# Kernel tuning notes

Measured on AMD Instinct MI355X. Metric: run time of the kernel, lower is better.

The kernel has to match this reference:

```python
import jax, jax.numpy as jnp
import numpy as np

B, S, H, DH = 4, 2048, 16, 64
D = H * DH          # 1024
EXP = 2
FF_IN = EXP * D * 2  # 4096 (SwiGLU doubles)
FF_HID = EXP * D     # 2048
SCALE_BASE = 512
LN_EPS = 1e-5


def setup_inputs() -> dict:
    key = jax.random.key(0)
    ks = jax.random.split(key, 8)
    inp = {
        "q": jax.random.normal(ks[0], (B, S, D), jnp.float32),
        "k": jax.random.normal(ks[1], (B, S, D), jnp.float32),
        "v": jax.random.normal(ks[2], (B, S, D), jnp.float32),
        "Wqkv": jax.random.normal(ks[3], (D, 3 * D), jnp.float32) * (1.0 / np.sqrt(D)),
        "bqkv": jnp.zeros((3 * D,), jnp.float32),
        "q_scale": jnp.ones((DH,), jnp.float32),
        "k_scale": jnp.ones((DH,), jnp.float32),
        "ln_g": jnp.ones((D,), jnp.float32),
        "ln_b": jnp.zeros((D,), jnp.float32),
        "W1": jax.random.normal(ks[4], (D, FF_IN), jnp.float32) * (1.0 / np.sqrt(D)),
        "b1": jnp.zeros((FF_IN,), jnp.float32),
        "W2": jax.random.normal(ks[5], (FF_HID, D), jnp.float32) * (1.0 / np.sqrt(FF_HID)),
        "b2": jnp.zeros((D,), jnp.float32),
    }
    return inp


def rotate_half(x):
    x1, x2 = jnp.split(x, 2, axis=-1)
    return jnp.concatenate((-x2, x1), axis=-1)


def apply_rope(pos, t, scale):
    # pos: [S, DH], scale: [S, DH] (broadcast over [B, H, S, DH])
    return t * jnp.cos(pos) * scale + rotate_half(t) * jnp.sin(pos) * scale


def rotary_tables(seq_len):
    inv_freq = 1.0 / (10000.0 ** (jnp.arange(0, DH, 2, dtype=jnp.float32) / DH))
    t = jnp.arange(seq_len, dtype=jnp.float32)
    freqs = t[:, None] * inv_freq[None, :]            # [S, DH/2]
    freqs = jnp.concatenate((freqs, freqs), axis=-1)  # [S, DH]
    power = (t - seq_len // 2) / SCALE_BASE           # [S]
    base = (jnp.arange(0, DH, 2, dtype=jnp.float32) + 0.4 * DH) / (1.4 * DH)  # [DH/2]
    scale = base[None, :] ** power[:, None]           # [S, DH/2]
    scale = jnp.concatenate((scale, scale), axis=-1)  # [S, DH]
    return freqs, scale


def l2norm(x, eps=1e-12):
    n = jnp.sqrt(jnp.sum(x * x, axis=-1, keepdims=True))
    return x / jnp.maximum(n, eps)


def reference(q, k, v, Wqkv, bqkv, q_scale, k_scale, ln_g, ln_b, W1, b1, W2, b2):
    del k, v  # module projects qkv from q; k,v args are unused (faithful to source)
    n, seq_len, _ = q.shape
    qkv = q @ Wqkv + bqkv                              # [B, S, 3D]
    qkv = qkv.reshape(n, seq_len, H, 3 * DH).transpose(0, 2, 1, 3)  # [B, H, S, 3DH]
    q_, k_, v_ = jnp.split(qkv, 3, axis=-1)
    q_ = l2norm(q_) * q_scale
    k_ = l2norm(k_) * k_scale
    pos, xscale = rotary_tables(seq_len)
    q_ = apply_rope(pos, q_, xscale)
    k_ = apply_rope(pos, k_, 1.0 / xscale)
    # scaled dot product attention (non-causal)
    scores = jnp.einsum("bhid,bhjd->bhij", q_, k_) / np.sqrt(DH)
    attn = jax.nn.softmax(scores, axis=-1)
    out = jnp.einsum("bhij,bhjd->bhid", attn, v_)      # [B, H, S, DH]
    out = out.transpose(0, 2, 1, 3).reshape(n, seq_len, D)
    # LayerNorm
    mu = jnp.mean(out, axis=-1, keepdims=True)
    var = jnp.mean((out - mu) ** 2, axis=-1, keepdims=True)
    out = (out - mu) / jnp.sqrt(var + LN_EPS) * ln_g + ln_b
    # SwiGLU FFN (dropout = identity in eval)
    h = out @ W1 + b1                                  # [B, S, FF_IN]
    x_, gate = jnp.split(h, 2, axis=-1)
    ff = (jax.nn.silu(gate) * x_) @ W2 + b2            # [B, S, D]
    return out + ff
```

## Files before the change

kernel.cpp:

```cpp
#include <hip/hip_runtime.h>
#include <math.h>


typedef __bf16 bf16;
typedef bf16 bf16x8 __attribute__((ext_vector_type(8)));
typedef bf16 bf16x4 __attribute__((ext_vector_type(4)));
typedef float f32x4 __attribute__((ext_vector_type(4)));

#define MFMA(a, b, c) __builtin_amdgcn_mfma_f32_16x16x32_bf16(a, b, c, 0, 0, 0)

__device__ __forceinline__ void async16(const void* g, void* l) {
    __builtin_amdgcn_global_load_lds(
        (const __attribute__((address_space(1))) void*)g,
        (__attribute__((address_space(3))) void*)l,
        16, 0, 0);
}

__global__ __launch_bounds__(256) void fill_sentinel(float* __restrict__ o)
{
    size_t i = ((size_t)blockIdx.x * 256 + threadIdx.x) * 4;
    *(float4*)&o[i] = make_float4(0.25f, 0.25f, 0.25f, 0.25f);
}

__global__ __launch_bounds__(256) void convert_f32_bf16(
    const float* __restrict__ in, bf16* __restrict__ out)
{
    size_t i = ((size_t)blockIdx.x * 256 + threadIdx.x) * 8;
    float4 f0 = *(const float4*)&in[i];
    float4 f1 = *(const float4*)&in[i + 4];
    bf16x8 v;
    v[0] = (bf16)f0.x; v[1] = (bf16)f0.y; v[2] = (bf16)f0.z; v[3] = (bf16)f0.w;
    v[4] = (bf16)f1.x; v[5] = (bf16)f1.y; v[6] = (bf16)f1.z; v[7] = (bf16)f1.w;
    *(bf16x8*)&out[i] = v;
}

__global__ __launch_bounds__(256) void transpose_f32_bf16(
    const float* __restrict__ in, bf16* __restrict__ out, int K, int N)
{
    __shared__ bf16 T[64][70];
    const int tN = N >> 6;
    const int tk = blockIdx.x / tN, tn = blockIdx.x % tN;
    const int k0 = tk << 6, n0 = tn << 6;
    const int t = threadIdx.x;
    const int r = t >> 2, c0 = (t & 3) << 4;
    const float* src = &in[(size_t)(k0 + r) * N + n0 + c0];
    for (int j = 0; j < 4; ++j) {
        float4 f = *(const float4*)(src + 4 * j);
        T[r][c0 + 4 * j + 0] = (bf16)f.x;
        T[r][c0 + 4 * j + 1] = (bf16)f.y;
        T[r][c0 + 4 * j + 2] = (bf16)f.z;
        T[r][c0 + 4 * j + 3] = (bf16)f.w;
    }
    __syncthreads();
    bf16x8 o0, o1;
    for (int i = 0; i < 8; ++i) o0[i] = T[c0 + i][r];
    for (int i = 0; i < 8; ++i) o1[i] = T[c0 + 8 + i][r];
    *(bf16x8*)&out[(size_t)(n0 + r) * K + k0 + c0]     = o0;
    *(bf16x8*)&out[(size_t)(n0 + r) * K + k0 + c0 + 8] = o1;
}

__global__ __launch_bounds__(256) void transpose_v(
    const bf16* __restrict__ in, bf16* __restrict__ out)
{
    __shared__ bf16 T[64][72];
    const int bh = blockIdx.x >> 5;
    const int s0 = (blockIdx.x & 31) << 6;
    const bf16* ip = in + ((size_t)bh << 17) + (size_t)s0 * 64;
    bf16* op = out + ((size_t)bh << 17) + s0;
    const int t = threadIdx.x;
    const int r = t >> 2, c0 = (t & 3) << 4;
    *(bf16x8*)&T[r][c0]     = *(const bf16x8*)&ip[r * 64 + c0];
    *(bf16x8*)&T[r][c0 + 8] = *(const bf16x8*)&ip[r * 64 + c0 + 8];
    __syncthreads();
    bf16x8 o0, o1;
    for (int i = 0; i < 8; ++i) o0[i] = T[c0 + i][r];
    for (int i = 0; i < 8; ++i) o1[i] = T[c0 + 8 + i][r];
    *(bf16x8*)&op[(size_t)r * 2048 + c0]     = o0;
    *(bf16x8*)&op[(size_t)r * 2048 + c0 + 8] = o1;
}

template <int BN>
__device__ __forceinline__ void g256_stage(
    const bf16* __restrict__ Ag, const bf16* __restrict__ Bg, int kt,
    int lda, int K, char* aB, char* bB, int tid, int wave)
{
    for (int i = 0; i < 4; ++i) {
        int l = (i << 9) + tid;
        int r = l >> 3;
        int cbs = ((l & 7) ^ (r & 7)) << 3;
        int cu = (i << 9) + (wave << 6);
        async16(&Ag[(size_t)r * lda + kt + cbs], aB + (size_t)cu * 16);
    }
    for (int i = 0; i < BN / 64; ++i) {
        int l = (i << 9) + tid;
        int r = l >> 3;
        int cbs = ((l & 7) ^ (r & 7)) << 3;
        int cu = (i << 9) + (wave << 6);
        async16(&Bg[(size_t)r * K + kt + cbs], bB + (size_t)cu * 16);
    }
}

template <int NI>
__device__ __forceinline__ void g256_compute(
    const bf16* At, const bf16* Bt, f32x4 (&acc)[8][NI],
    int wm, int wn, int l16, int quad, int rsw)
{
    for (int kd = 0; kd < 2; ++kd) {
        bf16x8 af[8], bfr[NI];
        for (int mi = 0; mi < 8; ++mi) {
            int row = (wm << 7) + (mi << 4) + l16;
            af[mi] = *(const bf16x8*)&At[(row << 6) + ((((kd << 2) + quad) ^ rsw) << 3)];
        }
        for (int ni = 0; ni < NI; ++ni) {
            int row = wn * (NI << 4) + (ni << 4) + l16;
            bfr[ni] = *(const bf16x8*)&Bt[(row << 6) + ((((kd << 2) + quad) ^ rsw) << 3)];
        }
        __builtin_amdgcn_s_setprio(1);
        for (int mi = 0; mi < 8; ++mi)
            for (int ni = 0; ni < NI; ++ni)
                acc[mi][ni] = MFMA(af[mi], bfr[ni], acc[mi][ni]);
        __builtin_amdgcn_s_setprio(0);
    }
}

#define G256_WAIT()                                                        \
    if constexpr (BN == 256) asm volatile("s_waitcnt vmcnt(8)" ::: "memory"); \
    else                     asm volatile("s_waitcnt vmcnt(6)" ::: "memory")

template <int EPI, int BN>
__global__ __launch_bounds__(512, 2) void gemm256(
    const bf16* __restrict__ A, const bf16* __restrict__ BT,
    const float* __restrict__ bias, int M, int N, int K, int lda,
    bf16* __restrict__ C0, bf16* __restrict__ C1, bf16* __restrict__ C2,
    float* __restrict__ Cf, const bf16* __restrict__ resid)
{
    constexpr int NI = BN / 64;
    __shared__ bf16 As[2][256 * 64];
    __shared__ bf16 Bs[2][BN * 64];
    const int tid = threadIdx.x;
    const int lane = tid & 63, wave = tid >> 6;
    const int quad = lane >> 4, l16 = lane & 15;
    const int rsw = l16 & 7;
    const int wm = wave >> 2, wn = wave & 3;
    const int nb = N / BN;
    const int nwg = gridDim.x;
    const int bid = blockIdx.x;
    const int swz = (bid & 7) * (nwg >> 3) + (bid >> 3);
    const int bm = swz / nb, bn = swz % nb;
    const int m0 = bm << 8, n0 = bn * BN;
    const bf16* Ag = A + (size_t)m0 * lda;
    const bf16* Bg = BT + (size_t)n0 * K;
    char* a0 = (char*)&As[0][0]; char* a1 = (char*)&As[1][0];
    char* b0 = (char*)&Bs[0][0]; char* b1 = (char*)&Bs[1][0];

    f32x4 acc[8][NI] = {};
    const int NT = K >> 6;

    g256_stage<BN>(Ag, Bg, 0,  lda, K, a0, b0, tid, wave);
    g256_stage<BN>(Ag, Bg, 64, lda, K, a1, b1, tid, wave);
    G256_WAIT();
    __builtin_amdgcn_s_barrier();

    for (int t = 0; t < NT; t += 2) {
        g256_compute<NI>(&As[0][0], &Bs[0][0], acc, wm, wn, l16, quad, rsw);
        asm volatile("" ::: "memory");
        __builtin_amdgcn_s_barrier();
        if (t + 2 < NT) {
            g256_stage<BN>(Ag, Bg, (t + 2) << 6, lda, K, a0, b0, tid, wave);
            G256_WAIT();
        } else {
            asm volatile("s_waitcnt vmcnt(0)" ::: "memory");
        }
        __builtin_amdgcn_s_barrier();
        g256_compute<NI>(&As[1][0], &Bs[1][0], acc, wm, wn, l16, quad, rsw);
        asm volatile("" ::: "memory");
        __builtin_amdgcn_s_barrier();
        if (t + 3 < NT) {
            g256_stage<BN>(Ag, Bg, (t + 3) << 6, lda, K, a1, b1, tid, wave);
            G256_WAIT();
        } else {
            asm volatile("s_waitcnt vmcnt(0)" ::: "memory");
        }
        __builtin_amdgcn_s_barrier();
    }

    for (int mi = 0; mi < 8; ++mi) {
        for (int ni = 0; ni < NI; ++ni) {
            for (int r = 0; r < 4; ++r) {
                int row = m0 + (wm << 7) + (mi << 4) + (quad << 2) + r;
                int col = n0 + wn * (NI << 4) + (ni << 4) + l16;
                float v = acc[mi][ni][r] + bias[col];
                if (EPI == 0) {
                    int b = row >> 11, s = row & 2047;
                    int h = col / 192, w = col % 192;
                    int tq = w >> 6, d = w & 63;
                    bf16* dst = (tq == 0) ? C0 : (tq == 1) ? C1 : C2;
                    dst[((((size_t)b * 16 + h) * 2048 + s) << 6) + d] = (bf16)v;
                } else if (EPI == 1) {
                    C0[(size_t)row * N + col] = (bf16)v;
                } else {
                    float rv = (float)resid[(size_t)row * N + col];
                    Cf[(size_t)row * N + col] = v + rv;
                }
            }
        }
    }
}

__global__ __launch_bounds__(256) void norm_rope(
    bf16* __restrict__ qb, bf16* __restrict__ kb,
    const float* __restrict__ qs, const float* __restrict__ ks)
{
    const int wave = threadIdx.x >> 6, lane = threadIdx.x & 63;
    const int rid = blockIdx.x * 4 + wave;
    const bool is_k = rid >= 131072;
    const int idx = is_k ? rid - 131072 : rid;
    const int s = idx & 2047;
    bf16* ptr = (is_k ? kb : qb) + ((size_t)idx << 6);
    const int d = lane;

    float v = (float)ptr[d];
    float ss = v * v;
    for (int o = 1; o < 64; o <<= 1) ss += __shfl_xor(ss, o);
    float t = v * rsqrtf(fmaxf(ss, 1e-24f));
    t *= (is_k ? ks : qs)[d];

    float partner = __shfl_xor(t, 32);
    float rh = (d < 32) ? -partner : partner;

    const float fi = (float)(d & 31);
    float inv_freq = __builtin_amdgcn_exp2f(fi * -0.4152410118609203f);
    float pos = (float)s * inv_freq;
    float rev = pos * 0.15915494309189535f;
    rev = rev - floorf(rev);
    float sn = __builtin_amdgcn_sinf(rev);
    float cs = __builtin_amdgcn_cosf(rev);
    float base = (2.0f * fi + 25.6f) * (1.0f / 89.6f);
    float power = ((float)s - 1024.0f) * (1.0f / 512.0f);
    if (is_k) power = -power;
    float xsc = __builtin_amdgcn_exp2f(power * __builtin_amdgcn_logf(base));
    ptr[d] = (bf16)((t * cs + rh * sn) * xsc);
}

__device__ __forceinline__ void attn_stage(
    const bf16* __restrict__ Kp, const bf16* __restrict__ Vp, int kt,
    char* kB, char* vB, int tid, int wave)
{
    for (int i = 0; i < 2; ++i) {
        int l = (i << 8) + tid;
        int r = l >> 3;
        int cbs = ((l & 7) ^ (r & 7)) << 3;
        int cu = (i << 8) + (wave << 6);
        async16(&Kp[(size_t)(kt + r) * 64 + cbs], kB + (size_t)cu * 16);
        async16(&Vp[(size_t)r * 2048 + kt + cbs], vB + (size_t)cu * 16);
    }
}

__global__ __launch_bounds__(256) void attn(
    const bf16* __restrict__ Q, const bf16* __restrict__ Kb,
    const bf16* __restrict__ VT, bf16* __restrict__ O)
{
    __shared__ bf16 Ks[2][64 * 64];
    __shared__ bf16 Vt[2][64 * 64];
    __shared__ bf16 Ps[4][2][16][64];
    const int tid = threadIdx.x;
    const int lane = tid & 63, wave = tid >> 6;
    const int quad = lane >> 4, l16 = lane & 15;
    const int rsw = l16 & 7;
    const int bh = blockIdx.x >> 4;
    const int q0 = (blockIdx.x & 15) << 7;
    const int s_base = q0 + (wave << 5);
    const bf16* Qp = Q + ((size_t)bh << 17);
    const bf16* Kp = Kb + ((size_t)bh << 17);
    const bf16* Vp = VT + ((size_t)bh << 17);

    bf16x8 qf[2][2];
    for (int sub = 0; sub < 2; ++sub) {
        const bf16* qrow = Qp + (size_t)(s_base + (sub << 4) + l16) * 64;
        qf[sub][0] = *(const bf16x8*)&qrow[(quad << 3)];
        qf[sub][1] = *(const bf16x8*)&qrow[32 + (quad << 3)];
        for (int j = 0; j < 8; ++j) {
            qf[sub][0][j] = (bf16)((float)qf[sub][0][j] * 0.1803368801f);
            qf[sub][1][j] = (bf16)((float)qf[sub][1][j] * 0.1803368801f);
        }
    }
    bf16x8 ones = {};
    if (l16 == 0) for (int j = 0; j < 8; ++j) ones[j] = (bf16)1.0f;

    f32x4 oacc[2][4] = {};
    f32x4 lacc[2] = {};

    attn_stage(Kp, Vp, 0, (char*)&Ks[0][0], (char*)&Vt[0][0], tid, wave);

    int buf = 0;
    for (int kt = 0; kt < 2048; kt += 64, buf ^= 1) {
        __syncthreads();
        if (kt + 64 < 2048)
            attn_stage(Kp, Vp, kt + 64,
                       (char*)&Ks[buf ^ 1][0], (char*)&Vt[buf ^ 1][0], tid, wave);

        const bf16* Kt_ = &Ks[buf][0];
        const bf16* Vc_ = &Vt[buf][0];

        f32x4 sc[2][4];
        __builtin_amdgcn_s_setprio(1);
        for (int nt = 0; nt < 4; ++nt) {
            int row = (nt << 4) + l16;
            bf16x8 kf0 = *(const bf16x8*)&Kt_[(row << 6) + ((quad ^ rsw) << 3)];
            bf16x8 kf1 = *(const bf16x8*)&Kt_[(row << 6) + (((quad + 4) ^ rsw) << 3)];
            for (int sub = 0; sub < 2; ++sub) {
                f32x4 z = {};
                z = MFMA(kf0, qf[sub][0], z);
                z = MFMA(kf1, qf[sub][1], z);
                sc[sub][nt] = z;
            }
        }
        __builtin_amdgcn_s_setprio(0);

        for (int sub = 0; sub < 2; ++sub)
            for (int nt = 0; nt < 4; ++nt) {
                bf16x4 pk;
                for (int r = 0; r < 4; ++r)
                    pk[r] = (bf16)__builtin_amdgcn_exp2f(sc[sub][nt][r]);
                *(bf16x4*)&Ps[wave][sub][l16][(((nt << 2) + quad) ^ (rsw << 1)) << 2] = pk;
            }
        __builtin_amdgcn_wave_barrier();
        bf16x8 pf0[2], pf1[2];
        for (int sub = 0; sub < 2; ++sub) {
            pf0[sub] = *(const bf16x8*)&Ps[wave][sub][l16][(quad ^ rsw) << 3];
            pf1[sub] = *(const bf16x8*)&Ps[wave][sub][l16][((quad + 4) ^ rsw) << 3];
        }

        __builtin_amdgcn_s_setprio(1);
        for (int ntd = 0; ntd < 4; ++ntd) {
            int row = (ntd << 4) + l16;
            bf16x8 vf0 = *(const bf16x8*)&Vc_[(row << 6) + ((quad ^ rsw) << 3)];
            bf16x8 vf1 = *(const bf16x8*)&Vc_[(row << 6) + (((quad + 4) ^ rsw) << 3)];
            for (int sub = 0; sub < 2; ++sub) {
                oacc[sub][ntd] = MFMA(pf0[sub], vf0, oacc[sub][ntd]);
                oacc[sub][ntd] = MFMA(pf1[sub], vf1, oacc[sub][ntd]);
            }
        }
        for (int sub = 0; sub < 2; ++sub) {
            lacc[sub] = MFMA(pf0[sub], ones, lacc[sub]);
            lacc[sub] = MFMA(pf1[sub], ones, lacc[sub]);
        }
        __builtin_amdgcn_s_setprio(0);
    }

    const int b = bh >> 4, h = bh & 15;
    for (int sub = 0; sub < 2; ++sub)
        for (int r = 0; r < 4; ++r) {
            float l = __shfl(lacc[sub][r], quad << 4);
            float inv_l = 1.0f / l;
            int srow = s_base + (sub << 4) + (quad << 2) + r;
            for (int ntd = 0; ntd < 4; ++ntd) {
                int d = (ntd << 4) + l16;
                O[((((size_t)b * 2048 + srow) * 16) + h) * 64 + d] =
                    (bf16)(oacc[sub][ntd][r] * inv_l);
            }
        }
}

__global__ __launch_bounds__(256) void layernorm(
    const bf16* __restrict__ x, const float* __restrict__ g,
    const float* __restrict__ b, bf16* __restrict__ y)
{
    __shared__ float red[8];
    const int row = blockIdx.x;
    const int t = threadIdx.x;
    const bf16* xr = x + ((size_t)row << 10);
    bf16x4 xv = *(const bf16x4*)&xr[t << 2];
    float v[4], s = 0.0f, sq = 0.0f;
    for (int i = 0; i < 4; ++i) { v[i] = (float)xv[i]; s += v[i]; sq += v[i] * v[i]; }
    for (int o = 1; o < 64; o <<= 1) { s += __shfl_xor(s, o); sq += __shfl_xor(sq, o); }
    const int wave = t >> 6, lane = t & 63;
    if (lane == 0) { red[wave] = s; red[4 + wave] = sq; }
    __syncthreads();
    s  = red[0] + red[1] + red[2] + red[3];
    sq = red[4] + red[5] + red[6] + red[7];
    float mu = s * (1.0f / 1024.0f);
    float var = fmaxf(sq * (1.0f / 1024.0f) - mu * mu, 0.0f);
    float rstd = rsqrtf(var + 1e-5f);
    bf16x4 ov;
    for (int i = 0; i < 4; ++i) {
        int c = (t << 2) + i;
        ov[i] = (bf16)((v[i] - mu) * rstd * g[c] + b[c]);
    }
    *(bf16x4*)(y + ((size_t)row << 10) + (t << 2)) = ov;
}

__global__ __launch_bounds__(256) void swiglu(bf16* __restrict__ h)
{
    size_t i = ((size_t)blockIdx.x * 256 + threadIdx.x) * 8;
    size_t row = i >> 11, c = i & 2047;
    bf16* hr = h + (row << 12);
    bf16x8 xv = *(const bf16x8*)&hr[c];
    bf16x8 gv = *(const bf16x8*)&hr[c + 2048];
    bf16x8 ov;
    for (int j = 0; j < 8; ++j) {
        float xf = (float)xv[j], gf = (float)gv[j];
        ov[j] = (bf16)(gf / (1.0f + __expf(-gf)) * xf);
    }
    *(bf16x8*)&hr[c] = ov;
}

extern "C" void kernel_launch(void* const* d_in, const int* in_sizes, int n_in,
                              void* d_out, int out_size, void* d_ws, size_t ws_size,
                              hipStream_t stream) {
    (void)in_sizes; (void)n_in; (void)out_size;
    const float* q    = (const float*)d_in[0];
    const float* Wqkv = (const float*)d_in[3];
    const float* bqkv = (const float*)d_in[4];
    const float* qsc  = (const float*)d_in[5];
    const float* ksc  = (const float*)d_in[6];
    const float* lng  = (const float*)d_in[7];
    const float* lnb  = (const float*)d_in[8];
    const float* W1   = (const float*)d_in[9];
    const float* b1   = (const float*)d_in[10];
    const float* W2   = (const float*)d_in[11];
    const float* b2   = (const float*)d_in[12];
    float* out = (float*)d_out;

    const size_t MB = 1024 * 1024;
    if (ws_size < 92 * MB) {
        fill_sentinel<<<8192, 256, 0, stream>>>(out);
        return;
    }

    char* ws = (char*)d_ws;
    bf16* W2T      = (bf16*)(ws + 0);
    bf16* ln_buf   = (bf16*)(ws + 4  * MB);
    bf16* q_bf     = (bf16*)(ws + 4  * MB);
    bf16* W1T      = (bf16*)(ws + 20 * MB);
    bf16* q_buf    = (bf16*)(ws + 28 * MB);
    bf16* k_buf    = (bf16*)(ws + 44 * MB);
    bf16* v_buf    = (bf16*)(ws + 60 * MB);
    bf16* WqkvT    = (bf16*)(ws + 76 * MB);
    bf16* vt_buf   = (bf16*)(ws + 76 * MB);
    bf16* attn_buf = (bf16*)(ws + 60 * MB);
    bf16* h_buf    = (bf16*)(ws + 28 * MB);

    convert_f32_bf16<<<4096, 256, 0, stream>>>(q, q_bf);
    transpose_f32_bf16<<<512,  256, 0, stream>>>(W2,   W2T,   2048, 1024);
    transpose_f32_bf16<<<1024, 256, 0, stream>>>(W1,   W1T,   1024, 4096);
    transpose_f32_bf16<<<768,  256, 0, stream>>>(Wqkv, WqkvT, 1024, 3072);

    gemm256<0, 128><<<768, 512, 0, stream>>>(q_bf, WqkvT, bqkv, 8192, 3072, 1024, 1024,
                                             q_buf, k_buf, v_buf, nullptr, nullptr);
    norm_rope<<<65536, 256, 0, stream>>>(q_buf, k_buf, qsc, ksc);
    transpose_v<<<2048, 256, 0, stream>>>(v_buf, vt_buf);
    attn<<<1024, 256, 0, stream>>>(q_buf, k_buf, vt_buf, attn_buf);
    layernorm<<<8192, 256, 0, stream>>>(attn_buf, lng, lnb, ln_buf);
    gemm256<1, 256><<<512, 512, 0, stream>>>(ln_buf, W1T, b1, 8192, 4096, 1024, 1024,
                                             h_buf, nullptr, nullptr, nullptr, nullptr);
    swiglu<<<8192, 256, 0, stream>>>(h_buf);
    gemm256<2, 128><<<256, 512, 0, stream>>>(h_buf, W2T, b2, 8192, 1024, 2048, 4096,
                                             nullptr, nullptr, nullptr, out, ln_buf);
}
```

Before: 515.4 us.

## Keep attention probabilities in registers by permuting K rows to match MFMA layout

The per-wave LDS round trip for the softmax probabilities (store, wave barrier, reload) is removed. K rows are loaded in a permuted order so the score MFMA output lands directly in the register layout the PV MFMA expects as its A operand, and the exp2 results are packed straight into pf0/pf1. A new XOR swizzle (swz_a) is applied to both K and V tiles to keep LDS reads conflict-free under the new row access pattern. This cuts LDS traffic and one barrier per key tile, but the permutation must exactly match the MFMA operand layout or the results will be wrong.

After: 508.7 us. About the same (-1.3%).

```diff
diff --git a/kernel.cpp b/kernel.cpp
--- a/kernel.cpp
+++ b/kernel.cpp
@@ -242,6 +242,11 @@
     ptr[d] = (bf16)((t * cs + rh * sn) * xsc);
 }
 
+__device__ __forceinline__ int swz_a(int r) {
+    int a = (r >> 3) & 3;
+    return (r & 7) ^ a ^ ((a << 1) & 7);
+}
+
 __device__ __forceinline__ void attn_stage(
     const bf16* __restrict__ Kp, const bf16* __restrict__ Vp, int kt,
     char* kB, char* vB, int tid, int wave)
@@ -249,7 +254,7 @@
     for (int i = 0; i < 2; ++i) {
         int l = (i << 8) + tid;
         int r = l >> 3;
-        int cbs = ((l & 7) ^ (r & 7)) << 3;
+        int cbs = ((l & 7) ^ swz_a(r)) << 3;
         int cu = (i << 8) + (wave << 6);
         async16(&Kp[(size_t)(kt + r) * 64 + cbs], kB + (size_t)cu * 16);
         async16(&Vp[(size_t)r * 2048 + kt + cbs], vB + (size_t)cu * 16);
@@ -262,11 +267,9 @@
 {
     __shared__ bf16 Ks[2][64 * 64];
     __shared__ bf16 Vt[2][64 * 64];
-    __shared__ bf16 Ps[4][2][16][64];
     const int tid = threadIdx.x;
     const int lane = tid & 63, wave = tid >> 6;
     const int quad = lane >> 4, l16 = lane & 15;
-    const int rsw = l16 & 7;
     const int bh = blockIdx.x >> 4;
     const int q0 = (blockIdx.x & 15) << 7;
     const int s_base = q0 + (wave << 5);
@@ -302,40 +305,32 @@
         const bf16* Kt_ = &Ks[buf][0];
         const bf16* Vc_ = &Vt[buf][0];
 
-        f32x4 sc[2][4];
-        __builtin_amdgcn_s_setprio(1);
+        bf16x8 pf0[2], pf1[2];
         for (int nt = 0; nt < 4; ++nt) {
-            int row = (nt << 4) + l16;
-            bf16x8 kf0 = *(const bf16x8*)&Kt_[(row << 6) + ((quad ^ rsw) << 3)];
-            bf16x8 kf1 = *(const bf16x8*)&Kt_[(row << 6) + (((quad + 4) ^ rsw) << 3)];
+            const int g = ((l16 >> 2) << 3) + (l16 & 3)
+                        + ((nt & 1) << 2) + ((nt >> 1) << 5);
+            const int gs = swz_a(g);
+            bf16x8 kf0 = *(const bf16x8*)&Kt_[(g << 6) + ((quad ^ gs) << 3)];
+            bf16x8 kf1 = *(const bf16x8*)&Kt_[(g << 6) + (((quad + 4) ^ gs) << 3)];
+            __builtin_amdgcn_s_setprio(1);
             for (int sub = 0; sub < 2; ++sub) {
                 f32x4 z = {};
                 z = MFMA(kf0, qf[sub][0], z);
                 z = MFMA(kf1, qf[sub][1], z);
-                sc[sub][nt] = z;
+                bf16x8& dst = (nt < 2) ? pf0[sub] : pf1[sub];
+                const int jb = (nt & 1) << 2;
+                for (int r = 0; r < 4; ++r)
+                    dst[jb + r] = (bf16)__builtin_amdgcn_exp2f(z[r]);
             }
-        }
-        __builtin_amdgcn_s_setprio(0);
-
-        for (int sub = 0; sub < 2; ++sub)
-            for (int nt = 0; nt < 4; ++nt) {
-                bf16x4 pk;
-                for (int r = 0; r < 4; ++r)
-                    pk[r] = (bf16)__builtin_amdgcn_exp2f(sc[sub][nt][r]);
-                *(bf16x4*)&Ps[wave][sub][l16][(((nt << 2) + quad) ^ (rsw << 1)) << 2] = pk;
-            }
-        __builtin_amdgcn_wave_barrier();
-        bf16x8 pf0[2], pf1[2];
-        for (int sub = 0; sub < 2; ++sub) {
-            pf0[sub] = *(const bf16x8*)&Ps[wave][sub][l16][(quad ^ rsw) << 3];
-            pf1[sub] = *(const bf16x8*)&Ps[wave][sub][l16][((quad + 4) ^ rsw) << 3];
+            __builtin_amdgcn_s_setprio(0);
         }
 
         __builtin_amdgcn_s_setprio(1);
         for (int ntd = 0; ntd < 4; ++ntd) {
             int row = (ntd << 4) + l16;
-            bf16x8 vf0 = *(const bf16x8*)&Vc_[(row << 6) + ((quad ^ rsw) << 3)];
-            bf16x8 vf1 = *(const bf16x8*)&Vc_[(row << 6) + (((quad + 4) ^ rsw) << 3)];
+            int vs = swz_a(row);
+            bf16x8 vf0 = *(const bf16x8*)&Vc_[(row << 6) + ((quad ^ vs) << 3)];
+            bf16x8 vf1 = *(const bf16x8*)&Vc_[(row << 6) + (((quad + 4) ^ vs) << 3)];
             for (int sub = 0; sub < 2; ++sub) {
                 oacc[sub][ntd] = MFMA(pf0[sub], vf0, oacc[sub][ntd]);
                 oacc[sub][ntd] = MFMA(pf1[sub], vf1, oacc[sub][ntd]);
```
